# Optimization experiments

Hardware: AMD Instinct MI355X
Metric: run time of the kernel (lower is better)

Reference implementation:

```python
import jax, jax.numpy as jnp
import numpy as np
from jax import lax

K = 3       # kernel_size
STRIDE = 1
PAD = 1
DIL = 1


def setup_inputs() -> dict:
    key = jax.random.key(0)
    ks = jax.random.split(key, 4)
    B, Cin, Cout, H, W = 4, 128, 256, 64, 64
    x = jax.random.normal(ks[0], (B, Cin, H, W), jnp.float32)
    # offset/mask conv params: out channels = 3*K*K (groups=1). Small weights
    # keep predicted offsets within a few pixels (module inits them to zero).
    om_w = jax.random.normal(ks[1], (3 * K * K, Cin, K, K), jnp.float32) * 0.01
    om_b = jnp.zeros((3 * K * K,), jnp.float32)
    weight = jax.random.normal(ks[2], (Cout, Cin, K, K), jnp.float32) * (1.0 / np.sqrt(Cin * K * K))
    bias = jnp.zeros((Cout,), jnp.float32)
    return {"x": x, "om_w": om_w, "om_b": om_b, "weight": weight, "bias": bias}


def _deform_conv(x, om_w, om_b, weight, bias):
    B, Cin, H, W = x.shape
    Cout = weight.shape[0]
    kk = K * K

    # offset/mask conv (stride/pad/dilation same as main conv)
    om = lax.conv_general_dilated(
        x, om_w, (STRIDE, STRIDE), [(PAD, PAD), (PAD, PAD)],
        rhs_dilation=(DIL, DIL), dimension_numbers=('NCHW', 'OIHW', 'NCHW'))
    om = om + om_b[None, :, None, None]
    Ho, Wo = om.shape[2], om.shape[3]

    off = om[:, :2 * kk].reshape(B, 2, kk, Ho, Wo)
    off_x, off_y = off[:, 0], off[:, 1]           # [B,kk,Ho,Wo]
    mask = jax.nn.sigmoid(om[:, 2 * kk:])          # [B,kk,Ho,Wo]

    # base grid (output pixel -> input pixel of kernel center)
    gy, gx = jnp.meshgrid(jnp.arange(Ho, dtype=x.dtype), jnp.arange(Wo, dtype=x.dtype), indexing='ij')
    base_x = gx * STRIDE - PAD
    base_y = gy * STRIDE - PAD
    # kernel taps centered at 0: arange(-(K-1)//2, (K+1)//2)
    r = jnp.arange(-(K - 1) // 2, (K + 1) // 2, dtype=x.dtype)
    koy, kox = jnp.meshgrid(r * DIL, r * DIL, indexing='ij')
    kox = kox.reshape(kk, 1, 1)
    koy = koy.reshape(kk, 1, 1)

    sx = base_x[None, None] + kox[None] + off_x    # [B,kk,Ho,Wo]
    sy = base_y[None, None] + koy[None] + off_y

    # Faithful to original: coords normalized with align_corners=True formula
    # (2*s/(size-1)-1) but grid_sample called with align_corners=False, i.e.
    # pixel coord = ((g+1)*size - 1)/2  =>  s*size/(size-1) - 0.5
    ix = sx * (W / (W - 1.0)) - 0.5
    iy = sy * (H / (H - 1.0)) - 0.5

    x0 = jnp.floor(ix)
    y0 = jnp.floor(iy)
    x1 = x0 + 1.0
    y1 = y0 + 1.0
    wx1 = ix - x0
    wx0 = 1.0 - wx1
    wy1 = iy - y0
    wy0 = 1.0 - wy1

    img = x.reshape(B, Cin, H * W)

    def gather(yy, xx):
        yi = yy.astype(jnp.int32)
        xi = xx.astype(jnp.int32)
        valid = ((yi >= 0) & (yi < H) & (xi >= 0) & (xi < W)).astype(x.dtype)
        idx = jnp.clip(yi, 0, H - 1) * W + jnp.clip(xi, 0, W - 1)   # [B,kk,Ho,Wo]
        v = jax.vmap(lambda im, i: im[:, i])(img, idx.reshape(B, -1))  # [B,Cin,kk*Ho*Wo]
        return v.reshape(B, Cin, kk, Ho, Wo) * valid[:, None]

    # bilinear (zeros padding) sample at kk taps per output pixel
    sampled = (gather(y0, x0) * (wy0 * wx0)[:, None]
               + gather(y0, x1) * (wy0 * wx1)[:, None]
               + gather(y1, x0) * (wy1 * wx0)[:, None]
               + gather(y1, x1) * (wy1 * wx1)[:, None])   # [B,Cin,kk,Ho,Wo]

    sampled = sampled * mask[:, None]
    w = weight.reshape(Cout, Cin, kk)
    out = jnp.einsum('bckhw,ock->bohw', sampled, w)
    return out + bias[None, :, None, None]


def reference(x, om_w, om_b, weight, bias):
    return _deform_conv(x, om_w, om_b, weight, bias)
```

## Files before the change

### kernel.cpp

```cpp
#include <hip/hip_runtime.h>
#include <hip/hip_bf16.h>

typedef _Float16 h4 __attribute__((ext_vector_type(4)));
typedef _Float16 h8 __attribute__((ext_vector_type(8)));
typedef float f32x4 __attribute__((ext_vector_type(4)));

#define CIN 128
#define COUT 256
#define KDIM (CIN*9)

__global__ __launch_bounds__(256) void k_pt(const float* __restrict__ x,
                                            const float* __restrict__ wgt,
                                            const float* __restrict__ om_w,
                                            unsigned short* __restrict__ xT,
                                            unsigned short* __restrict__ Wf,
                                            unsigned short* __restrict__ omWf) {
    __shared__ unsigned short tile[64][132];
    const int bid = blockIdx.x;
    if (bid < 256) {
        const int b = bid >> 6, y = bid & 63;
        const float* xp = x + (size_t)b * CIN * 4096 + y * 64;
        const int w = threadIdx.x & 63, cg = threadIdx.x >> 6;
#pragma unroll
        for (int cc = 0; cc < CIN; cc += 4) {
            int c = cc + cg;
            _Float16 hv = (_Float16)xp[(size_t)c * 4096 + w];
            tile[w][c] = *(unsigned short*)&hv;
        }
        __syncthreads();
        unsigned short* orow = xT + (size_t)(b * 4096 + y * 64) * CIN;
#pragma unroll
        for (int i = 0; i < 8; ++i) {
            int j = threadIdx.x + i * 256;
            int w2 = j >> 5, c2 = (j & 31) * 4;
            ushort4 v = *(ushort4*)&tile[w2][c2];
            ((ushort4*)orow)[j] = v;
        }
    } else if (bid < 1408) {
        int g = (bid - 256) * 256 + threadIdx.x;
        int o = g / KDIM, rem = g - o * KDIM;
        int c = rem / 9, k = rem - c * 9;
        int kc = k * 128 + c;
        int kch = kc >> 5, j = kc & 31;
        int l = ((j >> 3) << 4) | (o & 15);
        int e = j & 7, of = o >> 4;
        int f = ((kch * 16 + of) * 64 + l) * 8 + e;
        _Float16 hv = (_Float16)wgt[g];
        Wf[f] = *(unsigned short*)&hv;
    } else {
        int f = (bid - 1408) * 256 + threadIdx.x;
        int e = f & 7, l = (f >> 3) & 63, of = (f >> 9) & 1, kch = f >> 10;
        int o = of * 16 + (l & 15);
        int c = (kch & 3) * 32 + (l >> 4) * 8 + e;
        int k = kch >> 2;
        float v = (o < 27) ? om_w[(size_t)o * KDIM + c * 9 + k] : 0.f;
        _Float16 hv = (_Float16)v;
        omWf[f] = *(unsigned short*)&hv;
    }
}

__global__ __launch_bounds__(256, 3) void k_fused(const unsigned short* __restrict__ xT_u,
                                                  const unsigned short* __restrict__ omWf_u,
                                                  const float* __restrict__ om_b,
                                                  const unsigned short* __restrict__ Wf_u,
                                                  const float* __restrict__ bias,
                                                  float* __restrict__ out) {
    const int bid = blockIdx.x;
    const int half = bid & 1, h = (bid >> 1) & 63, b = bid >> 7;
    const int p_base = half * 32;
    const int tid = threadIdx.x;
    const int wv = tid >> 6, lane = tid & 63;
    const int khalf = lane >> 4, lr = lane & 15;

    __shared__ int   s_off[4][288];
    __shared__ float s_wt[4][288];
    __shared__ h8    s_tile[2][32 * 8];
    __shared__ float red[2][32][28];

    const _Float16* xb = (const _Float16*)xT_u + (size_t)b * (4096 * CIN);

    {
        const h8* Af = (const h8*)omWf_u;
        const int pg = wv & 1, kh2 = wv >> 1;
        const int pl = pg * 16 + lr;
        const int p = p_base + pl;
        const int k0 = kh2 ? 5 : 0, k1 = kh2 ? 9 : 5;
        f32x4 acc0 = (f32x4){0.f, 0.f, 0.f, 0.f};
        f32x4 acc1 = (f32x4){0.f, 0.f, 0.f, 0.f};
        for (int k = k0; k < k1; ++k) {
            const int ky = k / 3, kx = k - ky * 3;
            const int y = h + ky - 1, xq = p + kx - 1;
            const bool valid = ((unsigned)y < 64u) && ((unsigned)xq < 64u);
            const _Float16* src = xb + ((y * 64 + xq) * CIN);
#pragma unroll
            for (int cg = 0; cg < 4; ++cg) {
                h8 bf = {};
                if (valid) bf = *(const h8*)(src + cg * 32 + khalf * 8);
                const int kch = k * 4 + cg;
                h8 a0 = Af[(kch * 2 + 0) * 64 + lane];
                h8 a1 = Af[(kch * 2 + 1) * 64 + lane];
                acc0 = __builtin_amdgcn_mfma_f32_16x16x32_f16(a0, bf, acc0, 0, 0, 0);
                acc1 = __builtin_amdgcn_mfma_f32_16x16x32_f16(a1, bf, acc1, 0, 0, 0);
            }
        }
#pragma unroll
        for (int r = 0; r < 4; ++r) {
            red[kh2][pl][khalf * 4 + r] = acc0[r];
            int row1 = 16 + khalf * 4 + r;
            if (row1 < 27) red[kh2][pl][row1] = acc1[r];
        }
    }
    __syncthreads();

    for (int e = tid; e < 288; e += 256) {
        int k = e >> 5, pl = e & 31;
        int p = p_base + pl;
        float offx = red[0][pl][k]      + red[1][pl][k]      + om_b[k];
        float offy = red[0][pl][9 + k]  + red[1][pl][9 + k]  + om_b[9 + k];
        float mv   = red[0][pl][18 + k] + red[1][pl][18 + k] + om_b[18 + k];
        float mask = 1.f / (1.f + __expf(-mv));
        int ky = k / 3, kx = k - ky * 3;
        const float SC = 64.f / 63.f;
        float ix = ((float)(p + kx - 2) + offx) * SC - 0.5f;
        float iy = ((float)(h + ky - 2) + offy) * SC - 0.5f;
        float fx0 = floorf(ix), fy0 = floorf(iy);
        float wx1 = ix - fx0, wx0 = 1.f - wx1;
        float wy1 = iy - fy0, wy0 = 1.f - wy1;
        int x0 = (int)fx0, y0 = (int)fy0;
        int x1 = x0 + 1, y1 = y0 + 1;
        bool vx0 = (unsigned)x0 < 64u, vx1 = (unsigned)x1 < 64u;
        bool vy0 = (unsigned)y0 < 64u, vy1 = (unsigned)y1 < 64u;
        int xc0 = min(max(x0, 0), 63), xc1 = min(max(x1, 0), 63);
        int yc0 = min(max(y0, 0), 63), yc1 = min(max(y1, 0), 63);
        s_off[0][e] = (yc0 * 64 + xc0) * CIN;
        s_off[1][e] = (yc0 * 64 + xc1) * CIN;
        s_off[2][e] = (yc1 * 64 + xc0) * CIN;
        s_off[3][e] = (yc1 * 64 + xc1) * CIN;
        s_wt[0][e] = (vy0 && vx0) ? wy0 * wx0 * mask : 0.f;
        s_wt[1][e] = (vy0 && vx1) ? wy0 * wx1 * mask : 0.f;
        s_wt[2][e] = (vy1 && vx0) ? wy1 * wx0 * mask : 0.f;
        s_wt[3][e] = (vy1 && vx1) ? wy1 * wx1 * mask : 0.f;
    }
    __syncthreads();

    const int p  = tid >> 3;
    const int ci = tid & 7;
    const h8* Wf8 = (const h8*)Wf_u;
    const int wslot = ci ^ (p & 7);

    f32x4 acc[4][2];
#pragma unroll
    for (int i = 0; i < 4; ++i)
#pragma unroll
        for (int j = 0; j < 2; ++j) acc[i][j] = (f32x4){0.f, 0.f, 0.f, 0.f};

    {
        const int e0 = p;
        const int cb = ci * 8;
        h8 v00 = *(const h8*)(xb + s_off[0][e0] + cb);
        h8 v01 = *(const h8*)(xb + s_off[1][e0] + cb);
        h8 v10 = *(const h8*)(xb + s_off[2][e0] + cb);
        h8 v11 = *(const h8*)(xb + s_off[3][e0] + cb);
        const float m00 = s_wt[0][e0], m01 = s_wt[1][e0], m10 = s_wt[2][e0], m11 = s_wt[3][e0];
        h8 pk;
#pragma unroll
        for (int j = 0; j < 8; ++j) {
            float r = m00 * (float)v00[j] + m01 * (float)v01[j]
                    + m10 * (float)v10[j] + m11 * (float)v11[j];
            pk[j] = (_Float16)r;
        }
        s_tile[0][p * 8 + wslot] = pk;
    }
    __syncthreads();

    for (int ch = 0; ch < 18; ++ch) {
        const int cur = ch & 1;
        const int nxt = ch + 1;

        h8 v00, v01, v10, v11;
        float m00, m01, m10, m11;
        if (nxt < 18) {
            const int kn = nxt >> 1;
            const int e = kn * 32 + p;
            const int cb = (nxt & 1) * 64 + ci * 8;
            v00 = *(const h8*)(xb + s_off[0][e] + cb);
            v01 = *(const h8*)(xb + s_off[1][e] + cb);
            v10 = *(const h8*)(xb + s_off[2][e] + cb);
            v11 = *(const h8*)(xb + s_off[3][e] + cb);
            m00 = s_wt[0][e]; m01 = s_wt[1][e]; m10 = s_wt[2][e]; m11 = s_wt[3][e];
        }

        const int k = ch >> 1, chalf = ch & 1;
#pragma unroll
        for (int ks = 0; ks < 2; ++ks) {
            const int kch = k * 4 + chalf * 2 + ks;
            h8 a[4];
#pragma unroll
            for (int i = 0; i < 4; ++i)
                a[i] = Wf8[(kch * 16 + wv * 4 + i) * 64 + lane];
            h8 bf[2];
#pragma unroll
            for (int pf = 0; pf < 2; ++pf) {
                const int row = pf * 16 + lr;
                bf[pf] = s_tile[cur][row * 8 + ((ks * 4 + khalf) ^ (row & 7))];
            }
#pragma unroll
            for (int i = 0; i < 4; ++i)
#pragma unroll
                for (int pf = 0; pf < 2; ++pf)
                    acc[i][pf] = __builtin_amdgcn_mfma_f32_16x16x32_f16(a[i], bf[pf], acc[i][pf], 0, 0, 0);
        }

        if (nxt < 18) {
            h8 pk;
#pragma unroll
            for (int j = 0; j < 8; ++j) {
                float r = m00 * (float)v00[j] + m01 * (float)v01[j]
                        + m10 * (float)v10[j] + m11 * (float)v11[j];
                pk[j] = (_Float16)r;
            }
            s_tile[cur ^ 1][p * 8 + wslot] = pk;
        }
        __syncthreads();
    }

    float* outb = out + (size_t)b * COUT * 4096 + h * 64 + p_base;
#pragma unroll
    for (int i = 0; i < 4; ++i) {
#pragma unroll
        for (int r = 0; r < 4; ++r) {
            const int o = wv * 64 + i * 16 + khalf * 4 + r;
            const float bo = bias[o];
            float* orow = outb + (size_t)o * 4096;
#pragma unroll
            for (int pf = 0; pf < 2; ++pf)
                orow[pf * 16 + lr] = acc[i][pf][r] + bo;
        }
    }
}

extern "C" void kernel_launch(void* const* d_in, const int* in_sizes, int n_in,
                              void* d_out, int out_size, void* d_ws, size_t ws_size,
                              hipStream_t stream) {
    const float* x    = (const float*)d_in[0];
    const float* om_w = (const float*)d_in[1];
    const float* om_b = (const float*)d_in[2];
    const float* wgt  = (const float*)d_in[3];
    const float* bias = (const float*)d_in[4];
    float* out = (float*)d_out;

    char* ws = (char*)d_ws;
    unsigned short* xT   = (unsigned short*)ws;
    unsigned short* Wf   = (unsigned short*)(ws + 4194304);
    unsigned short* omWf = (unsigned short*)(ws + 4194304 + 589824);

    k_pt   <<<1552, 256, 0, stream>>>(x, wgt, om_w, xT, Wf, omWf);
    k_fused<<<512, 256, 0, stream>>>(xT, omWf, om_b, Wf, bias, out);
}
```

Baseline: 44.73 us.

## Sample bilinear B-fragments directly in registers, dropping shared-memory tile and barriers

```diff
diff --git a/kernel.cpp b/kernel.cpp
--- a/kernel.cpp
+++ b/kernel.cpp
@@ -74,7 +74,6 @@
 
     __shared__ int   s_off[4][288];
     __shared__ float s_wt[4][288];
-    __shared__ h8    s_tile[2][32 * 8];
     __shared__ float red[2][32][28];
 
     const _Float16* xb = (const _Float16*)xT_u + (size_t)b * (4096 * CIN);
@@ -143,98 +142,52 @@
     }
     __syncthreads();
 
-    const int p  = tid >> 3;
-    const int ci = tid & 7;
-    const h8* Wf8 = (const h8*)Wf_u;
-    const int wslot = ci ^ (p & 7);
-
-    f32x4 acc[4][2];
-#pragma unroll
-    for (int i = 0; i < 4; ++i)
-#pragma unroll
-        for (int j = 0; j < 2; ++j) acc[i][j] = (f32x4){0.f, 0.f, 0.f, 0.f};
-
     {
-        const int e0 = p;
-        const int cb = ci * 8;
-        h8 v00 = *(const h8*)(xb + s_off[0][e0] + cb);
-        h8 v01 = *(const h8*)(xb + s_off[1][e0] + cb);
-        h8 v10 = *(const h8*)(xb + s_off[2][e0] + cb);
-        h8 v11 = *(const h8*)(xb + s_off[3][e0] + cb);
-        const float m00 = s_wt[0][e0], m01 = s_wt[1][e0], m10 = s_wt[2][e0], m11 = s_wt[3][e0];
-        h8 pk;
-#pragma unroll
-        for (int j = 0; j < 8; ++j) {
-            float r = m00 * (float)v00[j] + m01 * (float)v01[j]
-                    + m10 * (float)v10[j] + m11 * (float)v11[j];
-            pk[j] = (_Float16)r;
-        }
-        s_tile[0][p * 8 + wslot] = pk;
-    }
-    __syncthreads();
-
-    for (int ch = 0; ch < 18; ++ch) {
-        const int cur = ch & 1;
-        const int nxt = ch + 1;
-
-        h8 v00, v01, v10, v11;
-        float m00, m01, m10, m11;
-        if (nxt < 18) {
-            const int kn = nxt >> 1;
-            const int e = kn * 32 + p;
-            const int cb = (nxt & 1) * 64 + ci * 8;
-            v00 = *(const h8*)(xb + s_off[0][e] + cb);
-            v01 = *(const h8*)(xb + s_off[1][e] + cb);
-            v10 = *(const h8*)(xb + s_off[2][e] + cb);
-            v11 = *(const h8*)(xb + s_off[3][e] + cb);
-            m00 = s_wt[0][e]; m01 = s_wt[1][e]; m10 = s_wt[2][e]; m11 = s_wt[3][e];
-        }
-
-        const int k = ch >> 1, chalf = ch & 1;
-#pragma unroll
-        for (int ks = 0; ks < 2; ++ks) {
-            const int kch = k * 4 + chalf * 2 + ks;
-            h8 a[4];
-#pragma unroll
-            for (int i = 0; i < 4; ++i)
-                a[i] = Wf8[(kch * 16 + wv * 4 + i) * 64 + lane];
-            h8 bf[2];
-#pragma unroll
-            for (int pf = 0; pf < 2; ++pf) {
-                const int row = pf * 16 + lr;
-                bf[pf] = s_tile[cur][row * 8 + ((ks * 4 + khalf) ^ (row & 7))];
+        const int pg3 = wv & 1;
+        const int oh  = wv >> 1;
+        const int pl3 = pg3 * 16 + lr;
+        const h8* Wf8 = (const h8*)Wf_u;
+
+        f32x4 acc[8];
+#pragma unroll
+        for (int i = 0; i < 8; ++i) acc[i] = (f32x4){0.f, 0.f, 0.f, 0.f};
+
+#pragma unroll 1
+        for (int tap = 0; tap < 9; ++tap) {
+            const int e = tap * 32 + pl3;
+            const int o0 = s_off[0][e], o1 = s_off[1][e], o2 = s_off[2][e], o3 = s_off[3][e];
+            const float m0 = s_wt[0][e], m1 = s_wt[1][e], m2 = s_wt[2][e], m3 = s_wt[3][e];
+#pragma unroll 2
+            for (int kg = 0; kg < 4; ++kg) {
+                const int cb = kg * 32 + khalf * 8;
+                h8 v0 = *(const h8*)(xb + o0 + cb);
+                h8 v1 = *(const h8*)(xb + o1 + cb);
+                h8 v2 = *(const h8*)(xb + o2 + cb);
+                h8 v3 = *(const h8*)(xb + o3 + cb);
+                h8 pk;
+#pragma unroll
+                for (int j = 0; j < 8; ++j) {
+                    float r = m0 * (float)v0[j] + m1 * (float)v1[j]
+                            + m2 * (float)v2[j] + m3 * (float)v3[j];
+                    pk[j] = (_Float16)r;
+                }
+                const int kch = tap * 4 + kg;
+#pragma unroll
+                for (int i = 0; i < 8; ++i) {
+                    h8 a = Wf8[(kch * 16 + oh * 8 + i) * 64 + lane];
+                    acc[i] = __builtin_amdgcn_mfma_f32_16x16x32_f16(a, pk, acc[i], 0, 0, 0);
+                }
             }
-#pragma unroll
-            for (int i = 0; i < 4; ++i)
-#pragma unroll
-                for (int pf = 0; pf < 2; ++pf)
-                    acc[i][pf] = __builtin_amdgcn_mfma_f32_16x16x32_f16(a[i], bf[pf], acc[i][pf], 0, 0, 0);
-        }
-
-        if (nxt < 18) {
-            h8 pk;
-#pragma unroll
-            for (int j = 0; j < 8; ++j) {
-                float r = m00 * (float)v00[j] + m01 * (float)v01[j]
-                        + m10 * (float)v10[j] + m11 * (float)v11[j];
-                pk[j] = (_Float16)r;
+        }
+
+        float* outb = out + (size_t)b * COUT * 4096 + h * 64 + p_base + pg3 * 16 + lr;
+#pragma unroll
+        for (int i = 0; i < 8; ++i) {
+#pragma unroll
+            for (int r = 0; r < 4; ++r) {
+                const int o = (oh * 8 + i) * 16 + khalf * 4 + r;
+                outb[(size_t)o * 4096] = acc[i][r] + bias[o];
             }
-            s_tile[cur ^ 1][p * 8 + wslot] = pk;
-        }
-        __syncthreads();
-    }
-
-    float* outb = out + (size_t)b * COUT * 4096 + h * 64 + p_base;
-#pragma unroll
-    for (int i = 0; i < 4; ++i) {
-#pragma unroll
-        for (int r = 0; r < 4; ++r) {
-            const int o = wv * 64 + i * 16 + khalf * 4 + r;
-            const float bo = bias[o];
-            float* orow = outb + (size_t)o * 4096;
-#pragma unroll
-            for (int pf = 0; pf < 2; ++pf)
-                orow[pf * 16 + lr] = acc[i][pf][r] + bo;
         }
     }
 }
```

Result: slower. 97.32 us (+117.6%).
